# Optimization experiments

Measured on AMD Instinct MI355X. Metric: run time of the kernel, lower is better.

Reference implementation:

```python
import jax, jax.numpy as jnp
import numpy as np

B, S, D, H, DK, DV, DFF, L, V = 8, 1024, 256, 8, 32, 32, 1024, 4, 28
EPS = 1e-5
NEG = -1e9


def _ln(x, w, b):
    m = jnp.mean(x, axis=-1, keepdims=True)
    v = jnp.var(x, axis=-1, keepdims=True)
    return (x - m) * jax.lax.rsqrt(v + EPS) * w + b


def setup_inputs() -> dict:
    key = jax.random.key(0)
    ks = jax.random.split(key, 30)
    std = 0.02
    inp = {
        'input_ids': jax.random.randint(ks[0], (B, S), 0, V),
        'tok_embed': jax.random.normal(ks[1], (V, D), jnp.float32) * std,
        'pos_embed': jax.random.normal(ks[2], (S, D), jnp.float32) * std,
        'emb_ln_w': jnp.ones((D,), jnp.float32),
        'emb_ln_b': jnp.zeros((D,), jnp.float32),
        'Wq': jax.random.normal(ks[3], (L, D, H * DK), jnp.float32) * std,
        'bq': jnp.zeros((L, H * DK), jnp.float32),
        'Wk': jax.random.normal(ks[4], (L, D, H * DK), jnp.float32) * std,
        'bk': jnp.zeros((L, H * DK), jnp.float32),
        'Wv': jax.random.normal(ks[5], (L, D, H * DV), jnp.float32) * std,
        'bv': jnp.zeros((L, H * DV), jnp.float32),
        'Wo': jax.random.normal(ks[6], (L, H * DV, D), jnp.float32) * std,
        'bo': jnp.zeros((L, D), jnp.float32),
        'ln_w': jnp.ones((L, D), jnp.float32),
        'ln_b': jnp.zeros((L, D), jnp.float32),
        'W1': jax.random.normal(ks[7], (L, D, DFF), jnp.float32) * std,
        'b1': jnp.zeros((L, DFF), jnp.float32),
        'W2': jax.random.normal(ks[8], (L, DFF, D), jnp.float32) * std,
        'b2': jnp.zeros((L, D), jnp.float32),
        'ft1_w': jax.random.normal(ks[9], (D, D), jnp.float32) * std,
        'ft1_b': jnp.zeros((D,), jnp.float32),
        'ft2_w': jax.random.normal(ks[10], (D, D // 2), jnp.float32) * std,
        'ft2_b': jnp.zeros((D // 2,), jnp.float32),
        'cls_w': jax.random.normal(ks[11], (D // 2, 2), jnp.float32) * std,
        'cls_b': jnp.zeros((2,), jnp.float32),
    }
    return inp


def reference(input_ids, tok_embed, pos_embed, emb_ln_w, emb_ln_b,
              Wq, bq, Wk, bk, Wv, bv, Wo, bo, ln_w, ln_b,
              W1, b1, W2, b2, ft1_w, ft1_b, ft2_w, ft2_b, cls_w, cls_b):
    # Embedding: tok + pos, then LayerNorm
    x = tok_embed[input_ids] + pos_embed[jnp.arange(S)][None, :, :]
    x = _ln(x, emb_ln_w, emb_ln_b)
    # pad mask: True where key position is pad (token id 0); broadcast [B,1,1,S]
    pad = (input_ids == 0)[:, None, None, :]
    scale = 1.0 / np.sqrt(DK)
    for i in range(L):
        residual = x
        q = (x @ Wq[i] + bq[i]).reshape(B, S, H, DK).transpose(0, 2, 1, 3)
        k = (x @ Wk[i] + bk[i]).reshape(B, S, H, DK).transpose(0, 2, 1, 3)
        v = (x @ Wv[i] + bv[i]).reshape(B, S, H, DV).transpose(0, 2, 1, 3)
        scores = jnp.einsum('bhqd,bhkd->bhqk', q, k) * scale
        scores = jnp.where(pad, NEG, scores)
        attn = jax.nn.softmax(scores, axis=-1)
        ctx = jnp.einsum('bhqk,bhkd->bhqd', attn, v)
        ctx = ctx.transpose(0, 2, 1, 3).reshape(B, S, H * DV)
        x = _ln(ctx @ Wo[i] + bo[i] + residual, ln_w[i], ln_b[i])
        # FFN (note: original has NO residual/norm after FFN)
        x = jax.nn.relu(x @ W1[i] + b1[i]) @ W2[i] + b2[i]
    cls = x[:, 0, :]
    feat = jax.nn.relu(cls @ ft1_w + ft1_b) @ ft2_w + ft2_b  # dropout = eval no-op
    logits = feat @ cls_w + cls_b
    return logits, feat
```

## Files before the change

kernel.cpp:

```cpp
#include <hip/hip_runtime.h>
#include <math.h>

#define S_ 1024
#define D_ 256

typedef __attribute__((ext_vector_type(8))) _Float16 half8;
typedef __attribute__((ext_vector_type(4))) _Float16 half4;
typedef __attribute__((ext_vector_type(4))) float f32x4;
typedef __attribute__((ext_vector_type(4))) unsigned int u32x4;

__device__ __forceinline__ float wave_sum64(float x) {
    x += __shfl_xor(x, 32); x += __shfl_xor(x, 16); x += __shfl_xor(x, 8);
    x += __shfl_xor(x, 4);  x += __shfl_xor(x, 2);  x += __shfl_xor(x, 1);
    return x;
}

__device__ __forceinline__ unsigned int pk2h(float lo, float hi) {
    unsigned short a = __builtin_bit_cast(unsigned short, (_Float16)lo);
    unsigned short b = __builtin_bit_cast(unsigned short, (_Float16)hi);
    return (unsigned int)a | ((unsigned int)b << 16);
}

#define GLD16(gp, lp) __builtin_amdgcn_global_load_lds( \
    (const __attribute__((address_space(1))) void*)(gp), \
    (__attribute__((address_space(3))) void*)(lp), 16, 0, 0)

__global__ __launch_bounds__(256) void transpose_cvt(
    const float* __restrict__ src, _Float16* __restrict__ dst, int K, int N)
{
    __shared__ float tile[32][33];
    src += (size_t)blockIdx.z * K * N;
    dst += (size_t)blockIdx.z * K * N;
    const int bx = blockIdx.x * 32;
    const int by = blockIdx.y * 32;
    const int t = threadIdx.x;
    const int c = t & 31, r0 = t >> 5;
    #pragma unroll
    for (int j = 0; j < 4; ++j)
        tile[r0 + 8 * j][c] = src[(size_t)(by + r0 + 8 * j) * N + bx + c];
    __syncthreads();
    #pragma unroll
    for (int j = 0; j < 4; ++j)
        dst[(size_t)(bx + r0 + 8 * j) * K + by + c] = (_Float16)tile[c][r0 + 8 * j];
}

__global__ __launch_bounds__(256) void transpose_qkv(
    const float* __restrict__ Wq, const float* __restrict__ Wk,
    const float* __restrict__ Wv, _Float16* __restrict__ qkvT)
{
    __shared__ float tile[32][33];
    const int z = blockIdx.z, l = z / 3, m = z % 3;
    const float* src = (m == 0 ? Wq : (m == 1 ? Wk : Wv)) + (size_t)l * 65536;
    _Float16* dst = qkvT + (size_t)l * 196608 + (size_t)m * 65536;
    const int bx = blockIdx.x * 32;
    const int by = blockIdx.y * 32;
    const int t = threadIdx.x;
    const int c = t & 31, r0 = t >> 5;
    #pragma unroll
    for (int j = 0; j < 4; ++j)
        tile[r0 + 8 * j][c] = src[(size_t)(by + r0 + 8 * j) * 256 + bx + c];
    __syncthreads();
    #pragma unroll
    for (int j = 0; j < 4; ++j)
        dst[(size_t)(bx + r0 + 8 * j) * 256 + by + c] = (_Float16)tile[c][r0 + 8 * j];
}

__global__ __launch_bounds__(256) void pack_bias(
    const float* __restrict__ bq, const float* __restrict__ bk,
    const float* __restrict__ bv, float* __restrict__ bqkv)
{
    const int z = blockIdx.x, l = z / 3, m = z % 3;
    const float* s = (m == 0 ? bq : (m == 1 ? bk : bv)) + l * 256;
    bqkv[l * 768 + m * 256 + threadIdx.x] = s[threadIdx.x];
}

__global__ __launch_bounds__(256) void embed_ln_kernel(
    const int* __restrict__ ids, const float* __restrict__ tok,
    const float* __restrict__ pos, const float* __restrict__ w,
    const float* __restrict__ b, float* __restrict__ X, _Float16* __restrict__ Xh)
{
    const int wv_ = threadIdx.x >> 6, lane = threadIdx.x & 63;
    const int tokid = blockIdx.x * 4 + wv_;
    const int s = tokid & (S_ - 1);
    const int id = ids[tokid];
    float4 e = *(const float4*)&tok[id * D_ + lane * 4];
    float4 p = *(const float4*)&pos[s * D_ + lane * 4];
    float4 x = make_float4(e.x + p.x, e.y + p.y, e.z + p.z, e.w + p.w);
    float sum = x.x + x.y + x.z + x.w;
    float sq  = x.x * x.x + x.y * x.y + x.z * x.z + x.w * x.w;
    sum = wave_sum64(sum); sq = wave_sum64(sq);
    float mean = sum * (1.f / D_);
    float var  = sq * (1.f / D_) - mean * mean;
    float rs   = rsqrtf(var + 1e-5f);
    float4 wv = *(const float4*)&w[lane * 4];
    float4 bv = *(const float4*)&b[lane * 4];
    float4 o = make_float4((x.x - mean) * rs * wv.x + bv.x,
                           (x.y - mean) * rs * wv.y + bv.y,
                           (x.z - mean) * rs * wv.z + bv.z,
                           (x.w - mean) * rs * wv.w + bv.w);
    *(float4*)&X[(size_t)tokid * D_ + lane * 4] = o;
    half4 oh = { (_Float16)o.x, (_Float16)o.y, (_Float16)o.z, (_Float16)o.w };
    *(half4*)&Xh[(size_t)tokid * D_ + lane * 4] = oh;
}

__global__ __launch_bounds__(256) void ln_kernel(
    const float* __restrict__ Y, const float* __restrict__ w,
    const float* __restrict__ b, _Float16* __restrict__ Th)
{
    const int wv_ = threadIdx.x >> 6, lane = threadIdx.x & 63;
    const int tokid = blockIdx.x * 4 + wv_;
    const size_t base = (size_t)tokid * D_ + lane * 4;
    float4 x = *(const float4*)&Y[base];
    float sum = x.x + x.y + x.z + x.w;
    float sq  = x.x * x.x + x.y * x.y + x.z * x.z + x.w * x.w;
    sum = wave_sum64(sum); sq = wave_sum64(sq);
    float mean = sum * (1.f / D_);
    float var  = sq * (1.f / D_) - mean * mean;
    float rs   = rsqrtf(var + 1e-5f);
    float4 wv = *(const float4*)&w[lane * 4];
    float4 bv = *(const float4*)&b[lane * 4];
    half4 oh = { (_Float16)((x.x - mean) * rs * wv.x + bv.x),
                 (_Float16)((x.y - mean) * rs * wv.y + bv.y),
                 (_Float16)((x.z - mean) * rs * wv.z + bv.z),
                 (_Float16)((x.w - mean) * rs * wv.w + bv.w) };
    *(half4*)&Th[base] = oh;
}

template<int MODE>
__global__ __launch_bounds__(256) void gemm_f16(
    const _Float16* __restrict__ A, const _Float16* __restrict__ Bt,
    const float* __restrict__ bias, const float* __restrict__ res,
    float* __restrict__ Cf, _Float16* __restrict__ Ch,
    int K, int N)
{
    __shared__ _Float16 As[2][8192];
    const int t = threadIdx.x;
    const int wid = t >> 6, lane = t & 63;
    const int wr = wid >> 1, wc = wid & 1;
    const int m0 = blockIdx.x * 128, n0 = blockIdx.y * 64;
    const int li = lane & 15, lg = lane >> 4;
    const int srow = lane >> 3;
    const int scg = (lane & 7) ^ srow;

    f32x4 acc[4][2];
    const f32x4 zf = {0.f, 0.f, 0.f, 0.f};
    #pragma unroll
    for (int mr = 0; mr < 4; ++mr) { acc[mr][0] = zf; acc[mr][1] = zf; }

    const int KT = K >> 6;
    {
        const _Float16* Ab = A + (size_t)m0 * K;
        #pragma unroll
        for (int j = 0; j < 4; ++j) {
            int row = (wid * 4 + j) * 8 + srow;
            GLD16(Ab + (size_t)row * K + scg * 8, &As[0][(wid * 4 + j) * 512]);
        }
    }

    for (int kt = 0; kt < KT; ++kt) {
        const int cur = kt & 1;
        half8 bfr[2][2];
        #pragma unroll
        for (int nr = 0; nr < 2; ++nr) {
            const _Float16* bp = Bt + (size_t)(n0 + wc * 32 + nr * 16 + li) * K + kt * 64 + lg * 8;
            bfr[nr][0] = *(const half8*)bp;
            bfr[nr][1] = *(const half8*)(bp + 32);
        }
        if (kt + 1 < KT) {
            const _Float16* Ab = A + (size_t)m0 * K + (kt + 1) * 64;
            #pragma unroll
            for (int j = 0; j < 4; ++j) {
                int row = (wid * 4 + j) * 8 + srow;
                GLD16(Ab + (size_t)row * K + scg * 8, &As[cur ^ 1][(wid * 4 + j) * 512]);
            }
            asm volatile("s_waitcnt vmcnt(8)" ::: "memory");
        } else {
            asm volatile("s_waitcnt vmcnt(4)" ::: "memory");
        }
        __builtin_amdgcn_s_barrier();
        #pragma unroll
        for (int kk = 0; kk < 2; ++kk) {
            half8 af[4];
            #pragma unroll
            for (int mr = 0; mr < 4; ++mr) {
                int arow = wr * 64 + mr * 16 + li;
                int ablk = (kk * 4 + lg) ^ (li & 7);
                af[mr] = *(const half8*)&As[cur][arow * 64 + ablk * 8];
            }
            #pragma unroll
            for (int mr = 0; mr < 4; ++mr)
                #pragma unroll
                for (int nr = 0; nr < 2; ++nr)
                    acc[mr][nr] = __builtin_amdgcn_mfma_f32_16x16x32_f16(
                        af[mr], bfr[nr][kk], acc[mr][nr], 0, 0, 0);
        }
        __builtin_amdgcn_s_barrier();
    }

    #pragma unroll
    for (int nr = 0; nr < 2; ++nr) {
        const int n = n0 + wc * 32 + nr * 16 + li;
        const float bv = bias[n];
        #pragma unroll
        for (int mr = 0; mr < 4; ++mr) {
            #pragma unroll
            for (int r = 0; r < 4; ++r) {
                const int m = m0 + wr * 64 + mr * 16 + lg * 4 + r;
                float o = acc[mr][nr][r] + bv;
                if (MODE == 1) o = fmaxf(o, 0.f);
                if (MODE == 4) o += res[(size_t)m * N + n];
                if (MODE == 0 || MODE == 2 || MODE == 4) Cf[(size_t)m * N + n] = o;
                if (MODE == 1 || MODE == 2 || MODE == 3) Ch[(size_t)m * N + n] = (_Float16)o;
            }
        }
    }
}

__global__ __launch_bounds__(256, 4) void attn_f16_kernel(
    const _Float16* __restrict__ qkv, const int* __restrict__ ids,
    _Float16* __restrict__ ctxo)
{
    __shared__ unsigned int Vp[32 * 36];
    __shared__ float maskn[64];
    const int t = threadIdx.x;
    const int bh = blockIdx.x, b = bh >> 3, h = bh & 7;
    const int q0 = blockIdx.y * 64;
    const int wid = t >> 6;
    const int lane = t & 63;
    const int i = lane & 15;
    const int g = lane >> 4;
    const int kp = t >> 3;
    const int v0s = (t & 7) * 4;

    const size_t bS = (size_t)b * S_;
    const float scale = 0.17677669529663687f;

    const half8 qf = *(const half8*)(qkv + (bS + q0 + wid * 16 + i) * 768 + h * 32 + g * 8);

    float m = -INFINITY, l = 0.f;
    f32x4 cacc[2];
    const f32x4 zf = {0.f, 0.f, 0.f, 0.f};
    cacc[0] = zf; cacc[1] = zf;

    const _Float16* kbase = qkv + 256 + (bS + i) * 768 + h * 32 + g * 8;
    const _Float16* vbase = qkv + 512 + (bS + 2 * kp) * 768 + h * 32 + v0s;

    for (int kt = 0; kt < 16; ++kt) {
        const int k0 = kt * 64;
        {
            const ushort* vb = (const ushort*)(vbase + (size_t)k0 * 768);
            ushort4 a0 = *(const ushort4*)vb;
            ushort4 a1 = *(const ushort4*)(vb + 768);
            u32x4 wv;
            wv[0] = (unsigned)a0.x | ((unsigned)a1.x << 16);
            wv[1] = (unsigned)a0.y | ((unsigned)a1.y << 16);
            wv[2] = (unsigned)a0.z | ((unsigned)a1.z << 16);
            wv[3] = (unsigned)a0.w | ((unsigned)a1.w << 16);
            *(u32x4*)&Vp[kp * 36 + v0s] = wv;
            if (t < 64) maskn[t] = (ids[bS + k0 + t] == 0) ? -1e9f : 0.f;
        }
        half8 kf[4];
        const _Float16* kb = kbase + (size_t)k0 * 768;
        #pragma unroll
        for (int c = 0; c < 4; ++c) kf[c] = *(const half8*)(kb + c * 16 * 768);
        f32x4 sacc[4];
        #pragma unroll
        for (int c = 0; c < 4; ++c)
            sacc[c] = __builtin_amdgcn_mfma_f32_16x16x32_f16(kf[c], qf, zf, 0, 0, 0);
        __syncthreads();
        float p[4][4];
        float tmax = -INFINITY;
        #pragma unroll
        for (int c = 0; c < 4; ++c) {
            float4 ad = *(const float4*)&maskn[c * 16 + g * 4];
            p[c][0] = fmaf(sacc[c][0], scale, ad.x);
            p[c][1] = fmaf(sacc[c][1], scale, ad.y);
            p[c][2] = fmaf(sacc[c][2], scale, ad.z);
            p[c][3] = fmaf(sacc[c][3], scale, ad.w);
            tmax = fmaxf(tmax, fmaxf(fmaxf(p[c][0], p[c][1]), fmaxf(p[c][2], p[c][3])));
        }
        tmax = fmaxf(tmax, __shfl_xor(tmax, 16));
        tmax = fmaxf(tmax, __shfl_xor(tmax, 32));
        float mn  = fmaxf(m, tmax);
        float fac = __expf(m - mn);
        float psum = 0.f;
        #pragma unroll
        for (int c = 0; c < 4; ++c) {
            p[c][0] = __expf(p[c][0] - mn); p[c][1] = __expf(p[c][1] - mn);
            p[c][2] = __expf(p[c][2] - mn); p[c][3] = __expf(p[c][3] - mn);
            psum += (p[c][0] + p[c][1]) + (p[c][2] + p[c][3]);
        }
        psum += __shfl_xor(psum, 16);
        psum += __shfl_xor(psum, 32);
        l = l * fac + psum;
        m = mn;
        cacc[0] *= fac;
        cacc[1] *= fac;
        unsigned int wrd[4][2];
        #pragma unroll
        for (int c = 0; c < 4; ++c) {
            wrd[c][0] = pk2h(p[c][0], p[c][1]);
            wrd[c][1] = pk2h(p[c][2], p[c][3]);
        }
        #pragma unroll
        for (int kc = 0; kc < 2; ++kc) {
            u32x4 bw;
            #pragma unroll
            for (int j2 = 0; j2 < 4; ++j2) {
                int src = ((2 * (g & 1) + (j2 >> 1)) << 4) + i;
                unsigned int lo = (unsigned int)__shfl((int)wrd[2 * kc][j2 & 1], src);
                unsigned int hi = (unsigned int)__shfl((int)wrd[2 * kc + 1][j2 & 1], src);
                bw[j2] = (g >= 2) ? hi : lo;
            }
            half8 pf = __builtin_bit_cast(half8, bw);
            #pragma unroll
            for (int vh = 0; vh < 2; ++vh) {
                const unsigned int* vp = &Vp[(kc * 16 + g * 4) * 36 + vh * 16 + i];
                u32x4 vw;
                vw[0] = vp[0]; vw[1] = vp[36]; vw[2] = vp[72]; vw[3] = vp[108];
                half8 vfh = __builtin_bit_cast(half8, vw);
                cacc[vh] = __builtin_amdgcn_mfma_f32_16x16x32_f16(vfh, pf, cacc[vh], 0, 0, 0);
            }
        }
        __syncthreads();
    }
    const float inv = 1.f / l;
    _Float16* crow = ctxo + (bS + q0 + wid * 16 + i) * 256 + h * 32;
    #pragma unroll
    for (int vh = 0; vh < 2; ++vh) {
        half4 st;
        #pragma unroll
        for (int r = 0; r < 4; ++r) st[r] = (_Float16)(cacc[vh][r] * inv);
        *(half4*)&crow[vh * 16 + g * 4] = st;
    }
}

__global__ __launch_bounds__(256) void head1_kernel(
    const float* __restrict__ X, const float* __restrict__ ft1w,
    const float* __restrict__ ft1b, float* __restrict__ h1)
{
    __shared__ float clsS[8][256];
    __shared__ float ps[8][8][32];
    const int t = threadIdx.x;
    #pragma unroll
    for (int b = 0; b < 8; ++b) clsS[b][t] = X[(size_t)b * S_ * D_ + t];
    __syncthreads();
    const int n = t & 31, dg = t >> 5;
    const int gn = blockIdx.x * 32 + n;
    float s[8] = {};
    for (int dd = 0; dd < 32; ++dd) {
        int d = dg * 32 + dd;
        float w = ft1w[d * 256 + gn];
        #pragma unroll
        for (int b = 0; b < 8; ++b) s[b] = fmaf(clsS[b][d], w, s[b]);
    }
    #pragma unroll
    for (int b = 0; b < 8; ++b) ps[dg][b][n] = s[b];
    __syncthreads();
    {
        const int b = t >> 5, nn = t & 31;
        float a = 0.f;
        #pragma unroll
        for (int g = 0; g < 8; ++g) a += ps[g][b][nn];
        const int gn2 = blockIdx.x * 32 + nn;
        h1[b * 256 + gn2] = fmaxf(a + ft1b[gn2], 0.f);
    }
}

__global__ __launch_bounds__(256) void head2_kernel(
    const float* __restrict__ h1, const float* __restrict__ ft2w,
    const float* __restrict__ ft2b, float* __restrict__ featW,
    float* __restrict__ out)
{
    __shared__ float hS[8][256];
    __shared__ float ps[8][8][32];
    const int t = threadIdx.x;
    #pragma unroll
    for (int b = 0; b < 8; ++b) hS[b][t] = h1[b * 256 + t];
    __syncthreads();
    const int n = t & 31, dg = t >> 5;
    const int gn = blockIdx.x * 32 + n;
    float s[8] = {};
    for (int dd = 0; dd < 32; ++dd) {
        int d = dg * 32 + dd;
        float w = ft2w[d * 128 + gn];
        #pragma unroll
        for (int b = 0; b < 8; ++b) s[b] = fmaf(hS[b][d], w, s[b]);
    }
    #pragma unroll
    for (int b = 0; b < 8; ++b) ps[dg][b][n] = s[b];
    __syncthreads();
    {
        const int b = t >> 5, nn = t & 31;
        float a = 0.f;
        #pragma unroll
        for (int g = 0; g < 8; ++g) a += ps[g][b][nn];
        const int gn2 = blockIdx.x * 32 + nn;
        float v = a + ft2b[gn2];
        featW[b * 128 + gn2] = v;
        out[16 + b * 128 + gn2] = v;
    }
}

__global__ __launch_bounds__(64) void head3_kernel(
    const float* __restrict__ featW, const float* __restrict__ clw,
    const float* __restrict__ clb, float* __restrict__ out)
{
    const int t = threadIdx.x;
    if (t < 16) {
        const int b = t >> 1, c = t & 1;
        float s = 0.f;
        for (int d = 0; d < 128; ++d) s = fmaf(featW[b * 128 + d], clw[d * 2 + c], s);
        out[t] = s + clb[c];
    }
}

extern "C" void kernel_launch(void* const* d_in, const int* in_sizes, int n_in,
                              void* d_out, int out_size, void* d_ws, size_t ws_size,
                              hipStream_t stream)
{
    const int*   ids  = (const int*)d_in[0];
    const float* tok  = (const float*)d_in[1];
    const float* pos  = (const float*)d_in[2];
    const float* elnw = (const float*)d_in[3];
    const float* elnb = (const float*)d_in[4];
    const float* Wq   = (const float*)d_in[5];
    const float* bq   = (const float*)d_in[6];
    const float* Wk   = (const float*)d_in[7];
    const float* bk   = (const float*)d_in[8];
    const float* Wv   = (const float*)d_in[9];
    const float* bv   = (const float*)d_in[10];
    const float* Wo   = (const float*)d_in[11];
    const float* bo   = (const float*)d_in[12];
    const float* lnw  = (const float*)d_in[13];
    const float* lnb  = (const float*)d_in[14];
    const float* W1   = (const float*)d_in[15];
    const float* b1   = (const float*)d_in[16];
    const float* W2   = (const float*)d_in[17];
    const float* b2   = (const float*)d_in[18];
    const float* ft1w = (const float*)d_in[19];
    const float* ft1b = (const float*)d_in[20];
    const float* ft2w = (const float*)d_in[21];
    const float* ft2b = (const float*)d_in[22];
    const float* clw  = (const float*)d_in[23];
    const float* clb  = (const float*)d_in[24];
    float* out = (float*)d_out;

    char* ws = (char*)d_ws;
    float*    X    = (float*)(ws);
    float*    Y    = (float*)(ws + (8ull << 20));
    _Float16* Xh   = (_Float16*)(ws + (16ull << 20));
    _Float16* Th   = (_Float16*)(ws + (20ull << 20));
    _Float16* qkvb = (_Float16*)(ws + (24ull << 20));
    _Float16* ctx  = (_Float16*)(ws + (36ull << 20));
    _Float16* Hb   = (_Float16*)(ws + (24ull << 20));
    _Float16* qkvT = (_Float16*)(ws + (40ull << 20));
    _Float16* WoT  = (_Float16*)(ws + (42ull << 20));
    _Float16* W1T  = (_Float16*)(ws + (43ull << 20));
    _Float16* W2T  = (_Float16*)(ws + (45ull << 20));
    float*    bqkv = (float*)(ws + (47ull << 20));
    float*    h1W  = (float*)(ws + (47ull << 20) + (16ull << 10));
    float*    feW  = (float*)(ws + (47ull << 20) + (24ull << 10));

    transpose_qkv<<<dim3(8, 8, 12), 256, 0, stream>>>(Wq, Wk, Wv, qkvT);
    transpose_cvt<<<dim3(8, 8, 4),  256, 0, stream>>>(Wo, WoT, 256, 256);
    transpose_cvt<<<dim3(32, 8, 4), 256, 0, stream>>>(W1, W1T, 256, 1024);
    transpose_cvt<<<dim3(8, 32, 4), 256, 0, stream>>>(W2, W2T, 1024, 256);
    pack_bias<<<12, 256, 0, stream>>>(bq, bk, bv, bqkv);

    embed_ln_kernel<<<2048, 256, 0, stream>>>(ids, tok, pos, elnw, elnb, X, Xh);

    for (int i = 0; i < 4; ++i) {
        gemm_f16<3><<<dim3(64, 12), 256, 0, stream>>>(
            Xh, qkvT + (size_t)i * 196608, bqkv + i * 768, nullptr, nullptr, qkvb, 256, 768);
        attn_f16_kernel<<<dim3(64, 16), 256, 0, stream>>>(qkvb, ids, ctx);
        gemm_f16<4><<<dim3(64, 4), 256, 0, stream>>>(
            ctx, WoT + (size_t)i * 65536, bo + i * 256, X, Y, nullptr, 256, 256);
        ln_kernel<<<2048, 256, 0, stream>>>(Y, lnw + i * 256, lnb + i * 256, Th);
        gemm_f16<1><<<dim3(64, 16), 256, 0, stream>>>(
            Th, W1T + (size_t)i * 262144, b1 + i * 1024, nullptr, nullptr, Hb, 256, 1024);
        gemm_f16<2><<<dim3(64, 4), 256, 0, stream>>>(
            Hb, W2T + (size_t)i * 262144, b2 + i * 256, nullptr, X, Xh, 1024, 256);
    }

    head1_kernel<<<8, 256, 0, stream>>>(X, ft1w, ft1b, h1W);
    head2_kernel<<<4, 256, 0, stream>>>(h1W, ft2w, ft2b, feW, out);
    head3_kernel<<<1, 64, 0, stream>>>(feW, clw, clb, out);
}
```

Before: 441.6 us.

## Transpose V in LDS and use 16x16x16 MFMA to avoid P shuffles

The attention kernel now stores V transposed in shared memory. P fragments can then feed a 16x16x16 f16 MFMA directly from each lane's score registers, which removes the cross-lane shuffles that repacked P for the x32 MFMA. It also folds log2(e) into the scale so it can use exp2f, and skips rescaling the accumulators when no lane's running max increases. The cost is that the MFMA count doubles at half the K depth, the transposed LDS stores are scattered and may cause bank conflicts, and the __any test adds a wave-wide branch.

```diff
diff --git a/kernel.cpp b/kernel.cpp
--- a/kernel.cpp
+++ b/kernel.cpp
@@ -6,6 +6,7 @@
 
 typedef __attribute__((ext_vector_type(8))) _Float16 half8;
 typedef __attribute__((ext_vector_type(4))) _Float16 half4;
+typedef __attribute__((ext_vector_type(2))) _Float16 half2v;
 typedef __attribute__((ext_vector_type(4))) float f32x4;
 typedef __attribute__((ext_vector_type(4))) unsigned int u32x4;
 
@@ -13,12 +14,6 @@
     x += __shfl_xor(x, 32); x += __shfl_xor(x, 16); x += __shfl_xor(x, 8);
     x += __shfl_xor(x, 4);  x += __shfl_xor(x, 2);  x += __shfl_xor(x, 1);
     return x;
-}
-
-__device__ __forceinline__ unsigned int pk2h(float lo, float hi) {
-    unsigned short a = __builtin_bit_cast(unsigned short, (_Float16)lo);
-    unsigned short b = __builtin_bit_cast(unsigned short, (_Float16)hi);
-    return (unsigned int)a | ((unsigned int)b << 16);
 }
 
 #define GLD16(gp, lp) __builtin_amdgcn_global_load_lds( \
@@ -220,7 +215,7 @@
     const _Float16* __restrict__ qkv, const int* __restrict__ ids,
     _Float16* __restrict__ ctxo)
 {
-    __shared__ unsigned int Vp[32 * 36];
+    __shared__ unsigned int VTp[32 * 36];
     __shared__ float maskn[64];
     const int t = threadIdx.x;
     const int bh = blockIdx.x, b = bh >> 3, h = bh & 7;
@@ -233,7 +228,7 @@
     const int v0s = (t & 7) * 4;
 
     const size_t bS = (size_t)b * S_;
-    const float scale = 0.17677669529663687f;
+    const float scale = 0.17677669529663687f * 1.4426950408889634f;
 
     const half8 qf = *(const half8*)(qkv + (bS + q0 + wid * 16 + i) * 768 + h * 32 + g * 8);
 
@@ -251,12 +246,10 @@
             const ushort* vb = (const ushort*)(vbase + (size_t)k0 * 768);
             ushort4 a0 = *(const ushort4*)vb;
             ushort4 a1 = *(const ushort4*)(vb + 768);
-            u32x4 wv;
-            wv[0] = (unsigned)a0.x | ((unsigned)a1.x << 16);
-            wv[1] = (unsigned)a0.y | ((unsigned)a1.y << 16);
-            wv[2] = (unsigned)a0.z | ((unsigned)a1.z << 16);
-            wv[3] = (unsigned)a0.w | ((unsigned)a1.w << 16);
-            *(u32x4*)&Vp[kp * 36 + v0s] = wv;
+            VTp[(v0s + 0) * 36 + kp] = (unsigned)a0.x | ((unsigned)a1.x << 16);
+            VTp[(v0s + 1) * 36 + kp] = (unsigned)a0.y | ((unsigned)a1.y << 16);
+            VTp[(v0s + 2) * 36 + kp] = (unsigned)a0.z | ((unsigned)a1.z << 16);
+            VTp[(v0s + 3) * 36 + kp] = (unsigned)a0.w | ((unsigned)a1.w << 16);
             if (t < 64) maskn[t] = (ids[bS + k0 + t] == 0) ? -1e9f : 0.f;
         }
         half8 kf[4];
@@ -281,45 +274,35 @@
         }
         tmax = fmaxf(tmax, __shfl_xor(tmax, 16));
         tmax = fmaxf(tmax, __shfl_xor(tmax, 32));
-        float mn  = fmaxf(m, tmax);
-        float fac = __expf(m - mn);
+        if (__any(tmax > m)) {
+            float mn  = fmaxf(m, tmax);
+            float fac = exp2f(m - mn);
+            l *= fac;
+            cacc[0] *= fac;
+            cacc[1] *= fac;
+            m = mn;
+        }
         float psum = 0.f;
         #pragma unroll
         for (int c = 0; c < 4; ++c) {
-            p[c][0] = __expf(p[c][0] - mn); p[c][1] = __expf(p[c][1] - mn);
-            p[c][2] = __expf(p[c][2] - mn); p[c][3] = __expf(p[c][3] - mn);
+            p[c][0] = exp2f(p[c][0] - m); p[c][1] = exp2f(p[c][1] - m);
+            p[c][2] = exp2f(p[c][2] - m); p[c][3] = exp2f(p[c][3] - m);
             psum += (p[c][0] + p[c][1]) + (p[c][2] + p[c][3]);
         }
         psum += __shfl_xor(psum, 16);
         psum += __shfl_xor(psum, 32);
-        l = l * fac + psum;
-        m = mn;
-        cacc[0] *= fac;
-        cacc[1] *= fac;
-        unsigned int wrd[4][2];
+        l += psum;
         #pragma unroll
         for (int c = 0; c < 4; ++c) {
-            wrd[c][0] = pk2h(p[c][0], p[c][1]);
-            wrd[c][1] = pk2h(p[c][2], p[c][3]);
-        }
-        #pragma unroll
-        for (int kc = 0; kc < 2; ++kc) {
-            u32x4 bw;
-            #pragma unroll
-            for (int j2 = 0; j2 < 4; ++j2) {
-                int src = ((2 * (g & 1) + (j2 >> 1)) << 4) + i;
-                unsigned int lo = (unsigned int)__shfl((int)wrd[2 * kc][j2 & 1], src);
-                unsigned int hi = (unsigned int)__shfl((int)wrd[2 * kc + 1][j2 & 1], src);
-                bw[j2] = (g >= 2) ? hi : lo;
-            }
-            half8 pf = __builtin_bit_cast(half8, bw);
+            half2v plo = __builtin_bit_cast(half2v, __builtin_amdgcn_cvt_pkrtz(p[c][0], p[c][1]));
+            half2v phi = __builtin_bit_cast(half2v, __builtin_amdgcn_cvt_pkrtz(p[c][2], p[c][3]));
+            half4 pb = { plo[0], plo[1], phi[0], phi[1] };
             #pragma unroll
             for (int vh = 0; vh < 2; ++vh) {
-                const unsigned int* vp = &Vp[(kc * 16 + g * 4) * 36 + vh * 16 + i];
-                u32x4 vw;
-                vw[0] = vp[0]; vw[1] = vp[36]; vw[2] = vp[72]; vw[3] = vp[108];
-                half8 vfh = __builtin_bit_cast(half8, vw);
-                cacc[vh] = __builtin_amdgcn_mfma_f32_16x16x32_f16(vfh, pf, cacc[vh], 0, 0, 0);
+                const unsigned int* vp = &VTp[(vh * 16 + i) * 36 + 8 * c + 2 * g];
+                unsigned long long vv = *(const unsigned long long*)vp;
+                half4 vf = __builtin_bit_cast(half4, vv);
+                cacc[vh] = __builtin_amdgcn_mfma_f32_16x16x16f16(vf, pb, cacc[vh], 0, 0, 0);
             }
         }
         __syncthreads();
```

Result: no change. 446.7 us (+1.2%).
